# Kernel tuning notes

Measured on AMD Instinct MI355X. Metric: run time of the kernel, lower is better.

Reference implementation:

```python
import jax, jax.numpy as jnp
import numpy as np

B, N, D = 2, 2048, 1024
H, DH = 16, 64
EPS = 1e-5


def _layernorm(t, g, b):
    m = jnp.mean(t, axis=-1, keepdims=True)
    v = jnp.mean(jnp.square(t - m), axis=-1, keepdims=True)
    return (t - m) * jax.lax.rsqrt(v + EPS) * g + b


def setup_inputs() -> dict:
    key = jax.random.key(0)
    ks = jax.random.split(key, 4)
    return {
        "x": jax.random.normal(ks[0], (B, N, D), dtype=jnp.float32),
        "ln_g": jnp.ones((D,), jnp.float32),
        "ln_b": jnp.zeros((D,), jnp.float32),
        "lnc_g": jnp.ones((D,), jnp.float32),
        "lnc_b": jnp.zeros((D,), jnp.float32),
        "Wq": jax.random.normal(ks[1], (D, H * DH), jnp.float32) * 0.02,
        "Wkv": jax.random.normal(ks[2], (D, 2 * H * DH), jnp.float32) * 0.02,
        "Wo": jax.random.normal(ks[3], (H * DH, D), jnp.float32) * 0.02,
    }


def reference(x, ln_g, ln_b, lnc_g, lnc_b, Wq, Wkv, Wo):
    scale = DH ** (-0.5)
    xn = _layernorm(x, ln_g, ln_b)          # self-attn: context = x
    cn = _layernorm(x, lnc_g, lnc_b)
    q = xn @ Wq                              # [b, n, h*d]
    kv = cn @ Wkv
    k, v = jnp.split(kv, 2, axis=-1)
    # b n (h d) -> b h n d
    q = q.reshape(B, N, H, DH).transpose(0, 2, 1, 3)
    k = k.reshape(B, N, H, DH).transpose(0, 2, 1, 3)
    v = v.reshape(B, N, H, DH).transpose(0, 2, 1, 3)
    sim = jnp.einsum("bhnd,bhmd->bhnm", q, k) * scale
    neg = -jnp.finfo(sim.dtype).max
    causal = jnp.tril(jnp.ones((N, N), dtype=bool))  # allow j <= i
    sim = jnp.where(causal[None, None], sim, neg)
    attn = jax.nn.softmax(sim.astype(jnp.float32), axis=-1)
    out = jnp.einsum("bhnm,bhmd->bhnd", attn, v)
    out = out.transpose(0, 2, 1, 3).reshape(B, N, H * DH)
    return out @ Wo
```

## Files before the change

kernel.cpp:

```cpp
#include <hip/hip_runtime.h>
#include <hip/hip_bf16.h>

#define B_  2
#define N_  2048
#define D_  1024
#define H_  16
#define DH_ 64
#define BN_ROWS (B_ * N_)
#define EPS_ 1e-5f
#define QKV_N 3072

typedef __attribute__((ext_vector_type(8))) short bf16x8_t;
typedef __attribute__((ext_vector_type(4))) float f32x4_t;

typedef const unsigned int __attribute__((address_space(1)))* gas_ptr;
typedef unsigned int __attribute__((address_space(3)))* las_ptr;

__device__ __forceinline__ void async16(const unsigned short* g, unsigned short* l) {
    __builtin_amdgcn_global_load_lds((gas_ptr)g, (las_ptr)l, 16, 0, 0);
}

__device__ __forceinline__ unsigned short f2bf(float f) {
    unsigned int u = __float_as_uint(f);
    unsigned int r = u + 0x7FFFu + ((u >> 16) & 1u);
    return (unsigned short)(r >> 16);
}

__device__ __forceinline__ unsigned int pk2bf(float a, float b) {
    __hip_bfloat162 t = __float22bfloat162_rn(float2{a, b});
    return *(unsigned int*)&t;
}

__global__ __launch_bounds__(256) void ln_wt_kernel(
    const float* __restrict__ x,
    const float* __restrict__ g1, const float* __restrict__ b1,
    const float* __restrict__ g2, const float* __restrict__ b2,
    const float* __restrict__ Wq, const float* __restrict__ Wkv,
    const float* __restrict__ Wo,
    unsigned short* __restrict__ xn, unsigned short* __restrict__ cn,
    unsigned short* __restrict__ wqkvT, unsigned short* __restrict__ woT) {
    const int bid = blockIdx.x;
    const int tid = threadIdx.x;

    if (bid < BN_ROWS) {
        const int row = bid;
        const float4 v = ((const float4*)(x + (size_t)row * D_))[tid];

        float s  = v.x + v.y + v.z + v.w;
        float s2 = v.x * v.x + v.y * v.y + v.z * v.z + v.w * v.w;
        #pragma unroll
        for (int off = 32; off > 0; off >>= 1) {
            s  += __shfl_down(s,  off);
            s2 += __shfl_down(s2, off);
        }
        __shared__ float red[8];
        if ((tid & 63) == 0) { red[tid >> 6] = s; red[4 + (tid >> 6)] = s2; }
        __syncthreads();
        const float S  = red[0] + red[1] + red[2] + red[3];
        const float S2 = red[4] + red[5] + red[6] + red[7];
        const float mean = S * (1.0f / D_);
        const float var  = S2 * (1.0f / D_) - mean * mean;
        const float rstd = rsqrtf(var + EPS_);

        const float4 G1 = ((const float4*)g1)[tid];
        const float4 B1 = ((const float4*)b1)[tid];
        const float4 G2 = ((const float4*)g2)[tid];
        const float4 B2 = ((const float4*)b2)[tid];

        float nx[4] = { (v.x - mean) * rstd, (v.y - mean) * rstd,
                        (v.z - mean) * rstd, (v.w - mean) * rstd };
        ushort4 o1, o2;
        o1.x = f2bf(nx[0] * G1.x + B1.x); o1.y = f2bf(nx[1] * G1.y + B1.y);
        o1.z = f2bf(nx[2] * G1.z + B1.z); o1.w = f2bf(nx[3] * G1.w + B1.w);
        o2.x = f2bf(nx[0] * G2.x + B2.x); o2.y = f2bf(nx[1] * G2.y + B2.y);
        o2.z = f2bf(nx[2] * G2.z + B2.z); o2.w = f2bf(nx[3] * G2.w + B2.w);
        ((ushort4*)(xn + (size_t)row * D_))[tid] = o1;
        ((ushort4*)(cn + (size_t)row * D_))[tid] = o2;
    } else {
        const int zz = bid - BN_ROWS;
        const float* src;
        unsigned short* dst;
        int N, t;
        if (zz < 1024)      { src = Wq;  dst = wqkvT;                       N = 1024; t = zz; }
        else if (zz < 3072) { src = Wkv; dst = wqkvT + (size_t)1024 * 1024; N = 2048; t = zz - 1024; }
        else                { src = Wo;  dst = woT;                         N = 1024; t = zz - 3072; }
        const int nb = N / 32;
        const int n0 = (t % nb) * 32, k0 = (t / nb) * 32;

        __shared__ float tile[32][33];
        const int tx = tid & 31, ty = tid >> 5;
        #pragma unroll
        for (int i = 0; i < 4; i++)
            tile[ty + i * 8][tx] = src[(size_t)(k0 + ty + i * 8) * N + n0 + tx];
        __syncthreads();
        #pragma unroll
        for (int i = 0; i < 4; i++)
            dst[(size_t)(n0 + ty + i * 8) * 1024 + k0 + tx] = f2bf(tile[tx][ty + i * 8]);
    }
}

template <int BM, bool FUSED, bool BF16OUT>
__global__ __launch_bounds__(256, 2) void gemm_kernel(
    const unsigned short* __restrict__ A0, const unsigned short* __restrict__ A1,
    const unsigned short* __restrict__ Bt, void* __restrict__ Cv,
    unsigned short* __restrict__ vt, int M, int N, int K) {
    constexpr int WM = BM / 2, MT = WM / 16, AI = BM / 32;
    __shared__ unsigned short As[BM * 64];
    __shared__ unsigned short Bs[128 * 64];
    const int tid = threadIdx.x, lane = tid & 63, w = tid >> 6;
    const int quad = lane >> 4, l16 = lane & 15;
    const int lr8 = lane >> 3, pg8 = lane & 7;
    const int wr = (w >> 1) * WM, wc = (w & 1) * 64;
    const int bm = blockIdx.y * BM, bn = blockIdx.x * 128;
    const unsigned short* A = (FUSED && bn >= 1024) ? A1 : A0;
    const float cscale = (FUSED && bn < 1024) ? 0.180336880111120f : 1.0f;

    f32x4_t acc[MT][4] = {};
    for (int k0 = 0; k0 < K; k0 += 64) {
        #pragma unroll
        for (int i = 0; i < AI; i++) {
            const int rb = w * (BM / 4) + i * 8;
            const int r  = rb + lr8;
            const int g  = pg8 ^ (r & 7);
            async16(&A[(size_t)(bm + r) * K + k0 + g * 8], &As[rb * 64]);
        }
        #pragma unroll
        for (int i = 0; i < 4; i++) {
            const int rb = w * 32 + i * 8;
            const int r  = rb + lr8;
            const int g  = pg8 ^ (r & 7);
            async16(&Bt[(size_t)(bn + r) * K + k0 + g * 8], &Bs[rb * 64]);
        }
        __syncthreads();
        #pragma unroll
        for (int kk = 0; kk < 64; kk += 32) {
            bf16x8_t af[MT], bfr[4];
            const int g0 = (kk >> 3) + quad;
            #pragma unroll
            for (int t = 0; t < MT; t++)
                af[t] = *(const bf16x8_t*)&As[(wr + t * 16 + l16) * 64 +
                                              ((g0 ^ (l16 & 7)) * 8)];
            #pragma unroll
            for (int t = 0; t < 4; t++)
                bfr[t] = *(const bf16x8_t*)&Bs[(wc + t * 16 + l16) * 64 +
                                               ((g0 ^ (l16 & 7)) * 8)];
            #pragma unroll
            for (int mt = 0; mt < MT; mt++)
                #pragma unroll
                for (int nt = 0; nt < 4; nt++)
                    acc[mt][nt] = __builtin_amdgcn_mfma_f32_16x16x32_bf16(
                        af[mt], bfr[nt], acc[mt][nt], 0, 0, 0);
        }
        __syncthreads();
    }

    if (FUSED && bn >= 2048) {
        const int seq0 = bm + wr;
        const int bq = seq0 >> 11;
        const int kt = (seq0 & (N_ - 1)) >> 6;
        #pragma unroll
        for (int nt = 0; nt < 4; nt++) {
            const int c = (bn - 2048) + wc + nt * 16 + l16;
            unsigned short* dst =
                vt + (((size_t)(bq * 32 + kt) * 1024) + c) * 64;
            #pragma unroll
            for (int mt = 0; mt < 4; mt++) {
                uint2 v2 = { pk2bf(acc[mt][nt][0], acc[mt][nt][1]),
                             pk2bf(acc[mt][nt][2], acc[mt][nt][3]) };
                *(uint2*)&dst[mt * 16 + quad * 4] = v2;
            }
        }
        return;
    }

    #pragma unroll
    for (int mt = 0; mt < MT; mt++)
        #pragma unroll
        for (int nt = 0; nt < 4; nt++)
            #pragma unroll
            for (int r = 0; r < 4; r++) {
                const int row = bm + wr + mt * 16 + quad * 4 + r;
                const int col = bn + wc + nt * 16 + l16;
                if (BF16OUT)
                    ((unsigned short*)Cv)[(size_t)row * N + col] =
                        f2bf(acc[mt][nt][r] * cscale);
                else
                    ((float*)Cv)[(size_t)row * N + col] = acc[mt][nt][r];
            }
}

__global__ __launch_bounds__(256, 2) void flash_attn_kernel(
    const unsigned short* __restrict__ qkv, const unsigned short* __restrict__ vt,
    unsigned short* __restrict__ out) {
    __shared__ unsigned short Qs[64 * 64];
    __shared__ unsigned short Ks[2][64 * 64];
    __shared__ unsigned short Vts[2][64 * 64];
    __shared__ unsigned short Ps[4][16 * 72];

    const int tid = threadIdx.x, lane = tid & 63, w = tid >> 6;
    const int quad = lane >> 4, l16 = lane & 15;
    const int lr8 = lane >> 3, pg8 = lane & 7;
    const int bid = blockIdx.x;
    const int bh   = (bid & 7) * 4 + ((bid >> 3) & 3);
    const int pair = bid >> 5;
    const int b = bh >> 4, h = bh & 15;

    const unsigned short* qb  = qkv + (size_t)(b * N_) * QKV_N + h * DH_;
    const unsigned short* kb  = qb + 1024;
    const unsigned short* vtb = vt + ((size_t)(b * 32) * 1024 + h * 64) * 64;

    bf16x8_t ones;
    #pragma unroll
    for (int j = 0; j < 8; j++) ones[j] = (short)0x3F80;

    for (int phase = 0; phase < 2; phase++) {
        const int qt = phase ? (31 - pair) : pair;
        const int qs = qt * 64;
        const int niter = qt + 1;

        __syncthreads();

        #pragma unroll
        for (int i = 0; i < 2; i++) {
            const int rb = w * 16 + i * 8;
            const int r  = rb + lr8;
            const int g  = pg8 ^ (r & 7);
            async16(&qb[(size_t)(qs + r) * QKV_N + g * 8], &Qs[rb * 64]);
            async16(&kb[(size_t)r * QKV_N + g * 8], &Ks[0][rb * 64]);
            async16(&vtb[(size_t)r * 64 + g * 8],   &Vts[0][rb * 64]);
        }

        f32x4_t o[4] = {};
        f32x4_t lacc = {};
        bf16x8_t qf[2];

        for (int jt = 0; jt < niter; jt++) {
            __syncthreads();

            if (jt + 1 < niter) {
                const int js = (jt + 1) * 64;
                const int bsel = (jt + 1) & 1;
                #pragma unroll
                for (int i = 0; i < 2; i++) {
                    const int rb = w * 16 + i * 8;
                    const int r  = rb + lr8;
                    const int g  = pg8 ^ (r & 7);
                    async16(&kb[(size_t)(js + r) * QKV_N + g * 8], &Ks[bsel][rb * 64]);
                    async16(&vtb[((size_t)(jt + 1) * 1024 + r) * 64 + g * 8],
                            &Vts[bsel][rb * 64]);
                }
            }
            const int buf = jt & 1;
            const int js = jt * 64;

            if (jt == 0) {
                #pragma unroll
                for (int k2 = 0; k2 < 2; k2++) {
                    const int g0 = k2 * 4 + quad;
                    qf[k2] = *(const bf16x8_t*)&Qs[
                        (w * 16 + l16) * 64 + (g0 ^ (l16 & 7)) * 8];
                }
            }

            f32x4_t s[4] = {};
            #pragma unroll
            for (int k2 = 0; k2 < 2; k2++) {
                const int g0 = k2 * 4 + quad;
                #pragma unroll
                for (int kt = 0; kt < 4; kt++) {
                    const bf16x8_t a = *(const bf16x8_t*)&Ks[buf][
                        (kt * 16 + l16) * 64 + (g0 ^ (l16 & 7)) * 8];
                    s[kt] = __builtin_amdgcn_mfma_f32_16x16x32_bf16(
                        a, qf[k2], s[kt], 0, 0, 0);
                }
            }

            const bool edge = (jt == niter - 1);
            #pragma unroll
            for (int kt = 0; kt < 4; kt++) {
                float p[4];
                #pragma unroll
                for (int r = 0; r < 4; r++) {
                    float sv = s[kt][r];
                    if (edge) {
                        const int key = js + kt * 16 + quad * 4 + r;
                        const int qy  = qs + w * 16 + l16;
                        if (key > qy) sv = -3e38f;
                    }
                    p[r] = exp2f(sv);
                }
                uint2 pk = { pk2bf(p[0], p[1]), pk2bf(p[2], p[3]) };
                *(uint2*)&Ps[w][l16 * 72 + kt * 16 + quad * 4] = pk;
            }

            #pragma unroll
            for (int k2 = 0; k2 < 2; k2++) {
                const int g0 = k2 * 4 + quad;
                const bf16x8_t ap = *(const bf16x8_t*)&Ps[w][
                    l16 * 72 + k2 * 32 + quad * 8];
                #pragma unroll
                for (int nt = 0; nt < 4; nt++) {
                    const bf16x8_t bv = *(const bf16x8_t*)&Vts[buf][
                        (nt * 16 + l16) * 64 + (g0 ^ (l16 & 7)) * 8];
                    o[nt] = __builtin_amdgcn_mfma_f32_16x16x32_bf16(
                        ap, bv, o[nt], 0, 0, 0);
                }
                lacc = __builtin_amdgcn_mfma_f32_16x16x32_bf16(
                    ap, ones, lacc, 0, 0, 0);
            }
        }

        #pragma unroll
        for (int r = 0; r < 4; r++) {
            const float inv = 1.0f / lacc[r];
            const int query = qs + w * 16 + quad * 4 + r;
            const int row = b * N_ + query;
            #pragma unroll
            for (int nt = 0; nt < 4; nt++) {
                const int col = h * DH_ + nt * 16 + l16;
                out[(size_t)row * (H_ * DH_) + col] = f2bf(o[nt][r] * inv);
            }
        }
    }
}

extern "C" void kernel_launch(void* const* d_in, const int* in_sizes, int n_in,
                              void* d_out, int out_size, void* d_ws, size_t ws_size,
                              hipStream_t stream) {
    const float* x     = (const float*)d_in[0];
    const float* ln_g  = (const float*)d_in[1];
    const float* ln_b  = (const float*)d_in[2];
    const float* lnc_g = (const float*)d_in[3];
    const float* lnc_b = (const float*)d_in[4];
    const float* Wq    = (const float*)d_in[5];
    const float* Wkv   = (const float*)d_in[6];
    const float* Wo    = (const float*)d_in[7];

    char* ws = (char*)d_ws;
    const size_t MB = 1024 * 1024;
    unsigned short* qkv   = (unsigned short*)(ws + 0 * MB);
    unsigned short* vtbuf = (unsigned short*)(ws + 24 * MB);
    unsigned short* xn    = (unsigned short*)(ws + 32 * MB);
    unsigned short* cn    = (unsigned short*)(ws + 40 * MB);
    unsigned short* wqkvT = (unsigned short*)(ws + 48 * MB);
    unsigned short* woT   = (unsigned short*)(ws + 54 * MB);
    unsigned short* ao    = xn;

    ln_wt_kernel<<<8192, 256, 0, stream>>>(
        x, ln_g, ln_b, lnc_g, lnc_b, Wq, Wkv, Wo, xn, cn, wqkvT, woT);

    gemm_kernel<128, true, true>
        <<<dim3(QKV_N / 128, BN_ROWS / 128), 256, 0, stream>>>(
        xn, cn, wqkvT, qkv, vtbuf, BN_ROWS, QKV_N, D_);

    flash_attn_kernel<<<B_ * H_ * 16, 256, 0, stream>>>(qkv, vtbuf, ao);

    gemm_kernel<64, false, false>
        <<<dim3(D_ / 128, BN_ROWS / 64), 256, 0, stream>>>(
        ao, nullptr, woT, (float*)d_out, nullptr, BN_ROWS, D_, H_ * DH_);
}
```

Before: 179.5 us.

## Split paired flash-attention query tiles into separate blocks, longest-first, and raise occupancy

The attention kernel no longer processes a balanced pair of query tiles per block. It now launches one block per query tile (1024 blocks) ordered from the longest causal row to the shortest, so the hardware scheduler does the load balancing. Per-thread LDS offsets and global pointers are precomputed outside the loop, and launch bounds go to 3 waves-per-SIMD target for attention and for the QKV GEMM. The higher minimum-occupancy hint may force register spills, and the shorter blocks pay more prologue overhead.

After: 182.8 us. About the same (+1.8%).

```diff
diff --git a/kernel.cpp b/kernel.cpp
--- a/kernel.cpp
+++ b/kernel.cpp
@@ -99,8 +99,8 @@
     }
 }
 
-template <int BM, bool FUSED, bool BF16OUT>
-__global__ __launch_bounds__(256, 2) void gemm_kernel(
+template <int BM, bool FUSED, bool BF16OUT, int MINW>
+__global__ __launch_bounds__(256, MINW) void gemm_kernel(
     const unsigned short* __restrict__ A0, const unsigned short* __restrict__ A1,
     const unsigned short* __restrict__ Bt, void* __restrict__ Cv,
     unsigned short* __restrict__ vt, int M, int N, int K) {
@@ -189,7 +189,7 @@
             }
 }
 
-__global__ __launch_bounds__(256, 2) void flash_attn_kernel(
+__global__ __launch_bounds__(256, 3) void flash_attn_kernel(
     const unsigned short* __restrict__ qkv, const unsigned short* __restrict__ vt,
     unsigned short* __restrict__ out) {
     __shared__ unsigned short Qs[64 * 64];
@@ -201,9 +201,12 @@
     const int quad = lane >> 4, l16 = lane & 15;
     const int lr8 = lane >> 3, pg8 = lane & 7;
     const int bid = blockIdx.x;
-    const int bh   = (bid & 7) * 4 + ((bid >> 3) & 3);
-    const int pair = bid >> 5;
+    const int b5  = bid & 31;
+    const int bh  = (b5 & 7) * 4 + (b5 >> 3);
+    const int qt  = 31 - (bid >> 5);
     const int b = bh >> 4, h = bh & 15;
+    const int qs = qt * 64;
+    const int niter = qt + 1;
 
     const unsigned short* qb  = qkv + (size_t)(b * N_) * QKV_N + h * DH_;
     const unsigned short* kb  = qb + 1024;
@@ -213,113 +216,109 @@
     #pragma unroll
     for (int j = 0; j < 8; j++) ones[j] = (short)0x3F80;
 
-    for (int phase = 0; phase < 2; phase++) {
-        const int qt = phase ? (31 - pair) : pair;
-        const int qs = qt * 64;
-        const int niter = qt + 1;
-
-        __syncthreads();
-
-        #pragma unroll
-        for (int i = 0; i < 2; i++) {
-            const int rb = w * 16 + i * 8;
-            const int r  = rb + lr8;
-            const int g  = pg8 ^ (r & 7);
-            async16(&qb[(size_t)(qs + r) * QKV_N + g * 8], &Qs[rb * 64]);
-            async16(&kb[(size_t)r * QKV_N + g * 8], &Ks[0][rb * 64]);
-            async16(&vtb[(size_t)r * 64 + g * 8],   &Vts[0][rb * 64]);
-        }
-
-        f32x4_t o[4] = {};
-        f32x4_t lacc = {};
-        bf16x8_t qf[2];
-
-        for (int jt = 0; jt < niter; jt++) {
-            __syncthreads();
-
-            if (jt + 1 < niter) {
-                const int js = (jt + 1) * 64;
-                const int bsel = (jt + 1) & 1;
-                #pragma unroll
-                for (int i = 0; i < 2; i++) {
-                    const int rb = w * 16 + i * 8;
-                    const int r  = rb + lr8;
-                    const int g  = pg8 ^ (r & 7);
-                    async16(&kb[(size_t)(js + r) * QKV_N + g * 8], &Ks[bsel][rb * 64]);
-                    async16(&vtb[((size_t)(jt + 1) * 1024 + r) * 64 + g * 8],
-                            &Vts[bsel][rb * 64]);
-                }
-            }
-            const int buf = jt & 1;
-            const int js = jt * 64;
-
-            if (jt == 0) {
-                #pragma unroll
-                for (int k2 = 0; k2 < 2; k2++) {
-                    const int g0 = k2 * 4 + quad;
-                    qf[k2] = *(const bf16x8_t*)&Qs[
-                        (w * 16 + l16) * 64 + (g0 ^ (l16 & 7)) * 8];
-                }
-            }
-
-            f32x4_t s[4] = {};
-            #pragma unroll
-            for (int k2 = 0; k2 < 2; k2++) {
-                const int g0 = k2 * 4 + quad;
-                #pragma unroll
-                for (int kt = 0; kt < 4; kt++) {
-                    const bf16x8_t a = *(const bf16x8_t*)&Ks[buf][
-                        (kt * 16 + l16) * 64 + (g0 ^ (l16 & 7)) * 8];
-                    s[kt] = __builtin_amdgcn_mfma_f32_16x16x32_bf16(
-                        a, qf[k2], s[kt], 0, 0, 0);
-                }
-            }
-
-            const bool edge = (jt == niter - 1);
+    const int r0 = w * 16 + lr8;
+    const int r1 = r0 + 8;
+    const int g0s = pg8 ^ (r0 & 7);
+    const int g1s = pg8 ^ (r1 & 7);
+    const unsigned short* kp0 = &kb[(size_t)r0 * QKV_N + g0s * 8];
+    const unsigned short* kp1 = &kb[(size_t)r1 * QKV_N + g1s * 8];
+    const unsigned short* vp0 = &vtb[(size_t)r0 * 64 + g0s * 8];
+    const unsigned short* vp1 = &vtb[(size_t)r1 * 64 + g1s * 8];
+    const int rb0 = w * 16, rb1 = w * 16 + 8;
+
+    async16(&qb[(size_t)(qs + r0) * QKV_N + g0s * 8], &Qs[rb0 * 64]);
+    async16(&qb[(size_t)(qs + r1) * QKV_N + g1s * 8], &Qs[rb1 * 64]);
+    async16(kp0, &Ks[0][rb0 * 64]);
+    async16(kp1, &Ks[0][rb1 * 64]);
+    async16(vp0, &Vts[0][rb0 * 64]);
+    async16(vp1, &Vts[0][rb1 * 64]);
+    __syncthreads();
+
+    bf16x8_t qf[2];
+    #pragma unroll
+    for (int k2 = 0; k2 < 2; k2++) {
+        const int gq = k2 * 4 + quad;
+        qf[k2] = *(const bf16x8_t*)&Qs[(w * 16 + l16) * 64 + ((gq ^ (l16 & 7)) * 8)];
+    }
+
+    int ksoff[2][4], vtoff[2][4], psoff[2];
+    #pragma unroll
+    for (int k2 = 0; k2 < 2; k2++) {
+        const int gq = k2 * 4 + quad;
+        #pragma unroll
+        for (int t = 0; t < 4; t++) {
+            ksoff[k2][t] = (t * 16 + l16) * 64 + ((gq ^ (l16 & 7)) * 8);
+            vtoff[k2][t] = ksoff[k2][t];
+        }
+        psoff[k2] = l16 * 72 + k2 * 32 + quad * 8;
+    }
+    const int qy = qs + w * 16 + l16;
+
+    f32x4_t o[4] = {};
+    f32x4_t lacc = {};
+
+    for (int jt = 0; jt < niter; jt++) {
+        if (jt) __syncthreads();
+
+        if (jt + 1 < niter) {
+            const size_t koff = (size_t)(jt + 1) * 64 * QKV_N;
+            const size_t voff = (size_t)(jt + 1) * 1024 * 64;
+            const int bsel = (jt + 1) & 1;
+            async16(kp0 + koff, &Ks[bsel][rb0 * 64]);
+            async16(kp1 + koff, &Ks[bsel][rb1 * 64]);
+            async16(vp0 + voff, &Vts[bsel][rb0 * 64]);
+            async16(vp1 + voff, &Vts[bsel][rb1 * 64]);
+        }
+        const int buf = jt & 1;
+        const int js = jt * 64;
+
+        f32x4_t s[4] = {};
+        #pragma unroll
+        for (int k2 = 0; k2 < 2; k2++)
             #pragma unroll
             for (int kt = 0; kt < 4; kt++) {
-                float p[4];
-                #pragma unroll
-                for (int r = 0; r < 4; r++) {
-                    float sv = s[kt][r];
-                    if (edge) {
-                        const int key = js + kt * 16 + quad * 4 + r;
-                        const int qy  = qs + w * 16 + l16;
-                        if (key > qy) sv = -3e38f;
-                    }
-                    p[r] = exp2f(sv);
-                }
-                uint2 pk = { pk2bf(p[0], p[1]), pk2bf(p[2], p[3]) };
-                *(uint2*)&Ps[w][l16 * 72 + kt * 16 + quad * 4] = pk;
-            }
-
-            #pragma unroll
-            for (int k2 = 0; k2 < 2; k2++) {
-                const int g0 = k2 * 4 + quad;
-                const bf16x8_t ap = *(const bf16x8_t*)&Ps[w][
-                    l16 * 72 + k2 * 32 + quad * 8];
-                #pragma unroll
-                for (int nt = 0; nt < 4; nt++) {
-                    const bf16x8_t bv = *(const bf16x8_t*)&Vts[buf][
-                        (nt * 16 + l16) * 64 + (g0 ^ (l16 & 7)) * 8];
-                    o[nt] = __builtin_amdgcn_mfma_f32_16x16x32_bf16(
-                        ap, bv, o[nt], 0, 0, 0);
-                }
-                lacc = __builtin_amdgcn_mfma_f32_16x16x32_bf16(
-                    ap, ones, lacc, 0, 0, 0);
-            }
-        }
-
-        #pragma unroll
-        for (int r = 0; r < 4; r++) {
-            const float inv = 1.0f / lacc[r];
-            const int query = qs + w * 16 + quad * 4 + r;
-            const int row = b * N_ + query;
+                const bf16x8_t a = *(const bf16x8_t*)&Ks[buf][ksoff[k2][kt]];
+                s[kt] = __builtin_amdgcn_mfma_f32_16x16x32_bf16(
+                    a, qf[k2], s[kt], 0, 0, 0);
+            }
+
+        const bool edge = (jt == niter - 1);
+        #pragma unroll
+        for (int kt = 0; kt < 4; kt++) {
+            float p[4];
+            #pragma unroll
+            for (int r = 0; r < 4; r++) {
+                float sv = s[kt][r];
+                if (edge && (js + kt * 16 + quad * 4 + r > qy)) sv = -3e38f;
+                p[r] = exp2f(sv);
+            }
+            uint2 pk = { pk2bf(p[0], p[1]), pk2bf(p[2], p[3]) };
+            *(uint2*)&Ps[w][l16 * 72 + kt * 16 + quad * 4] = pk;
+        }
+
+        #pragma unroll
+        for (int k2 = 0; k2 < 2; k2++) {
+            const bf16x8_t ap = *(const bf16x8_t*)&Ps[w][psoff[k2]];
             #pragma unroll
             for (int nt = 0; nt < 4; nt++) {
-                const int col = h * DH_ + nt * 16 + l16;
-                out[(size_t)row * (H_ * DH_) + col] = f2bf(o[nt][r] * inv);
-            }
+                const bf16x8_t bv = *(const bf16x8_t*)&Vts[buf][vtoff[k2][nt]];
+                o[nt] = __builtin_amdgcn_mfma_f32_16x16x32_bf16(
+                    ap, bv, o[nt], 0, 0, 0);
+            }
+            lacc = __builtin_amdgcn_mfma_f32_16x16x32_bf16(
+                ap, ones, lacc, 0, 0, 0);
+        }
+    }
+
+    #pragma unroll
+    for (int r = 0; r < 4; r++) {
+        const float inv = 1.0f / lacc[r];
+        const int query = qs + w * 16 + quad * 4 + r;
+        const int row = b * N_ + query;
+        #pragma unroll
+        for (int nt = 0; nt < 4; nt++) {
+            const int col = h * DH_ + nt * 16 + l16;
+            out[(size_t)row * (H_ * DH_) + col] = f2bf(o[nt][r] * inv);
         }
     }
 }
@@ -349,13 +348,13 @@
     ln_wt_kernel<<<8192, 256, 0, stream>>>(
         x, ln_g, ln_b, lnc_g, lnc_b, Wq, Wkv, Wo, xn, cn, wqkvT, woT);
 
-    gemm_kernel<128, true, true>
+    gemm_kernel<128, true, true, 3>
         <<<dim3(QKV_N / 128, BN_ROWS / 128), 256, 0, stream>>>(
         xn, cn, wqkvT, qkv, vtbuf, BN_ROWS, QKV_N, D_);
 
-    flash_attn_kernel<<<B_ * H_ * 16, 256, 0, stream>>>(qkv, vtbuf, ao);
-
-    gemm_kernel<64, false, false>
+    flash_attn_kernel<<<B_ * H_ * 32, 256, 0, stream>>>(qkv, vtbuf, ao);
+
+    gemm_kernel<64, false, false, 2>
         <<<dim3(D_ / 128, BN_ROWS / 64), 256, 0, stream>>>(
         ao, nullptr, woT, (float*)d_out, nullptr, BN_ROWS, D_, H_ * DH_);
 }
```

## Fold layernorm gain and bias into QKV weights and a bias vector

Applied to the files above, without the earlier changes.

The layernorm kernel now writes a single normalized activation without gain or bias, instead of two separate bf16 copies. The per-feature gains and the Q scale are folded into the transposed bf16 weights, and the bias terms become a per-output-column vector built with atomics and added in the QKV GEMM epilogue. This halves the normalized-activation writes and the A-operand traffic diversity, at the cost of a memset, atomics, and a bias load in the epilogue. Rounding changes because gains are applied to the weights before bf16 conversion.

After: 189.7 us. 5.7% more time.

```diff
diff --git a/kernel.cpp b/kernel.cpp
--- a/kernel.cpp
+++ b/kernel.cpp
@@ -9,6 +9,7 @@
 #define BN_ROWS (B_ * N_)
 #define EPS_ 1e-5f
 #define QKV_N 3072
+#define QSCALE 0.180336880111120f
 
 typedef __attribute__((ext_vector_type(8))) short bf16x8_t;
 typedef __attribute__((ext_vector_type(4))) float f32x4_t;
@@ -37,8 +38,9 @@
     const float* __restrict__ g2, const float* __restrict__ b2,
     const float* __restrict__ Wq, const float* __restrict__ Wkv,
     const float* __restrict__ Wo,
-    unsigned short* __restrict__ xn, unsigned short* __restrict__ cn,
-    unsigned short* __restrict__ wqkvT, unsigned short* __restrict__ woT) {
+    unsigned short* __restrict__ nrm,
+    unsigned short* __restrict__ wqkvT, unsigned short* __restrict__ woT,
+    float* __restrict__ bias) {
     const int bid = blockIdx.x;
     const int tid = threadIdx.x;
 
@@ -62,48 +64,67 @@
         const float var  = S2 * (1.0f / D_) - mean * mean;
         const float rstd = rsqrtf(var + EPS_);
 
-        const float4 G1 = ((const float4*)g1)[tid];
-        const float4 B1 = ((const float4*)b1)[tid];
-        const float4 G2 = ((const float4*)g2)[tid];
-        const float4 B2 = ((const float4*)b2)[tid];
-
-        float nx[4] = { (v.x - mean) * rstd, (v.y - mean) * rstd,
-                        (v.z - mean) * rstd, (v.w - mean) * rstd };
-        ushort4 o1, o2;
-        o1.x = f2bf(nx[0] * G1.x + B1.x); o1.y = f2bf(nx[1] * G1.y + B1.y);
-        o1.z = f2bf(nx[2] * G1.z + B1.z); o1.w = f2bf(nx[3] * G1.w + B1.w);
-        o2.x = f2bf(nx[0] * G2.x + B2.x); o2.y = f2bf(nx[1] * G2.y + B2.y);
-        o2.z = f2bf(nx[2] * G2.z + B2.z); o2.w = f2bf(nx[3] * G2.w + B2.w);
-        ((ushort4*)(xn + (size_t)row * D_))[tid] = o1;
-        ((ushort4*)(cn + (size_t)row * D_))[tid] = o2;
+        ushort4 o1;
+        o1.x = f2bf((v.x - mean) * rstd);
+        o1.y = f2bf((v.y - mean) * rstd);
+        o1.z = f2bf((v.z - mean) * rstd);
+        o1.w = f2bf((v.w - mean) * rstd);
+        ((ushort4*)(nrm + (size_t)row * D_))[tid] = o1;
     } else {
         const int zz = bid - BN_ROWS;
-        const float* src;
-        unsigned short* dst;
-        int N, t;
-        if (zz < 1024)      { src = Wq;  dst = wqkvT;                       N = 1024; t = zz; }
-        else if (zz < 3072) { src = Wkv; dst = wqkvT + (size_t)1024 * 1024; N = 2048; t = zz - 1024; }
-        else                { src = Wo;  dst = woT;                         N = 1024; t = zz - 3072; }
+        const float* src; unsigned short* dst;
+        const float* gv; const float* bv;
+        int N, t, boff; float cs;
+        if (zz < 1024) {
+            src = Wq;  dst = wqkvT;                       gv = g1; bv = b1;
+            N = 1024; t = zz;        cs = QSCALE; boff = 0;
+        } else if (zz < 3072) {
+            src = Wkv; dst = wqkvT + (size_t)1024 * 1024; gv = g2; bv = b2;
+            N = 2048; t = zz - 1024; cs = 1.0f;   boff = 1024;
+        } else {
+            src = Wo;  dst = woT;                         gv = nullptr; bv = nullptr;
+            N = 1024; t = zz - 3072; cs = 1.0f;   boff = 0;
+        }
         const int nb = N / 32;
         const int n0 = (t % nb) * 32, k0 = (t / nb) * 32;
 
         __shared__ float tile[32][33];
+        __shared__ float acc2[8][33];
         const int tx = tid & 31, ty = tid >> 5;
         #pragma unroll
         for (int i = 0; i < 4; i++)
             tile[ty + i * 8][tx] = src[(size_t)(k0 + ty + i * 8) * N + n0 + tx];
         __syncthreads();
+
+        const float gk = gv ? (gv[k0 + tx] * cs) : 1.0f;
         #pragma unroll
         for (int i = 0; i < 4; i++)
-            dst[(size_t)(n0 + ty + i * 8) * 1024 + k0 + tx] = f2bf(tile[tx][ty + i * 8]);
+            dst[(size_t)(n0 + ty + i * 8) * 1024 + k0 + tx] =
+                f2bf(tile[tx][ty + i * 8] * gk);
+
+        if (bv) {
+            float part = 0.0f;
+            #pragma unroll
+            for (int i = 0; i < 4; i++)
+                part += bv[k0 + ty + i * 8] * tile[ty + i * 8][tx];
+            acc2[ty][tx] = part;
+            __syncthreads();
+            if (ty == 0) {
+                float ssum = 0.0f;
+                #pragma unroll
+                for (int j = 0; j < 8; j++) ssum += acc2[j][tx];
+                atomicAdd(&bias[boff + n0 + tx], ssum * cs);
+            }
+        }
     }
 }
 
 template <int BM, bool FUSED, bool BF16OUT>
 __global__ __launch_bounds__(256, 2) void gemm_kernel(
-    const unsigned short* __restrict__ A0, const unsigned short* __restrict__ A1,
+    const unsigned short* __restrict__ A,
     const unsigned short* __restrict__ Bt, void* __restrict__ Cv,
-    unsigned short* __restrict__ vt, int M, int N, int K) {
+    unsigned short* __restrict__ vt, const float* __restrict__ bias,
+    int M, int N, int K) {
     constexpr int WM = BM / 2, MT = WM / 16, AI = BM / 32;
     __shared__ unsigned short As[BM * 64];
     __shared__ unsigned short Bs[128 * 64];
@@ -112,8 +133,6 @@
     const int lr8 = lane >> 3, pg8 = lane & 7;
     const int wr = (w >> 1) * WM, wc = (w & 1) * 64;
     const int bm = blockIdx.y * BM, bn = blockIdx.x * 128;
-    const unsigned short* A = (FUSED && bn >= 1024) ? A1 : A0;
-    const float cscale = (FUSED && bn < 1024) ? 0.180336880111120f : 1.0f;
 
     f32x4_t acc[MT][4] = {};
     for (int k0 = 0; k0 < K; k0 += 64) {
@@ -160,13 +179,15 @@
         const int kt = (seq0 & (N_ - 1)) >> 6;
         #pragma unroll
         for (int nt = 0; nt < 4; nt++) {
-            const int c = (bn - 2048) + wc + nt * 16 + l16;
+            const int col = bn + wc + nt * 16 + l16;
+            const float bb = bias[col];
+            const int c = col - 2048;
             unsigned short* dst =
                 vt + (((size_t)(bq * 32 + kt) * 1024) + c) * 64;
             #pragma unroll
             for (int mt = 0; mt < 4; mt++) {
-                uint2 v2 = { pk2bf(acc[mt][nt][0], acc[mt][nt][1]),
-                             pk2bf(acc[mt][nt][2], acc[mt][nt][3]) };
+                uint2 v2 = { pk2bf(acc[mt][nt][0] + bb, acc[mt][nt][1] + bb),
+                             pk2bf(acc[mt][nt][2] + bb, acc[mt][nt][3] + bb) };
                 *(uint2*)&dst[mt * 16 + quad * 4] = v2;
             }
         }
@@ -176,17 +197,19 @@
     #pragma unroll
     for (int mt = 0; mt < MT; mt++)
         #pragma unroll
-        for (int nt = 0; nt < 4; nt++)
+        for (int nt = 0; nt < 4; nt++) {
+            const int col = bn + wc + nt * 16 + l16;
+            const float bb = FUSED ? bias[col] : 0.0f;
             #pragma unroll
             for (int r = 0; r < 4; r++) {
                 const int row = bm + wr + mt * 16 + quad * 4 + r;
-                const int col = bn + wc + nt * 16 + l16;
                 if (BF16OUT)
                     ((unsigned short*)Cv)[(size_t)row * N + col] =
-                        f2bf(acc[mt][nt][r] * cscale);
+                        f2bf(acc[mt][nt][r] + bb);
                 else
                     ((float*)Cv)[(size_t)row * N + col] = acc[mt][nt][r];
             }
+        }
 }
 
 __global__ __launch_bounds__(256, 2) void flash_attn_kernel(
@@ -340,22 +363,24 @@
     const size_t MB = 1024 * 1024;
     unsigned short* qkv   = (unsigned short*)(ws + 0 * MB);
     unsigned short* vtbuf = (unsigned short*)(ws + 24 * MB);
-    unsigned short* xn    = (unsigned short*)(ws + 32 * MB);
-    unsigned short* cn    = (unsigned short*)(ws + 40 * MB);
+    unsigned short* nrm   = (unsigned short*)(ws + 32 * MB);
+    float*          bias  = (float*)         (ws + 40 * MB);
     unsigned short* wqkvT = (unsigned short*)(ws + 48 * MB);
     unsigned short* woT   = (unsigned short*)(ws + 54 * MB);
-    unsigned short* ao    = xn;
+    unsigned short* ao    = nrm;
+
+    hipMemsetAsync(bias, 0, QKV_N * sizeof(float), stream);
 
     ln_wt_kernel<<<8192, 256, 0, stream>>>(
-        x, ln_g, ln_b, lnc_g, lnc_b, Wq, Wkv, Wo, xn, cn, wqkvT, woT);
+        x, ln_g, ln_b, lnc_g, lnc_b, Wq, Wkv, Wo, nrm, wqkvT, woT, bias);
 
     gemm_kernel<128, true, true>
         <<<dim3(QKV_N / 128, BN_ROWS / 128), 256, 0, stream>>>(
-        xn, cn, wqkvT, qkv, vtbuf, BN_ROWS, QKV_N, D_);
+        nrm, wqkvT, qkv, vtbuf, bias, BN_ROWS, QKV_N, D_);
 
     flash_attn_kernel<<<B_ * H_ * 16, 256, 0, stream>>>(qkv, vtbuf, ao);
 
     gemm_kernel<64, false, false>
         <<<dim3(D_ / 128, BN_ROWS / 64), 256, 0, stream>>>(
-        ao, nullptr, woT, (float*)d_out, nullptr, BN_ROWS, D_, H_ * DH_);
-}
+        ao, woT, (float*)d_out, nullptr, nullptr, BN_ROWS, D_, H_ * DH_);
+}
```
